# Performance work log

Hardware: AMD Instinct MI355X
Metric: run time of the kernel (lower is better)

The kernel has to match this reference:

```python
import jax, jax.numpy as jnp
import numpy as np

N = 100000   # num_nodes
R = 8        # num_relations
D = 64       # hidden_dim
E = 3200000  # num_edges


def setup_inputs() -> dict:
    key = jax.random.key(0)
    ks = jax.random.split(key, 10)
    s = 1.0 / np.sqrt(D)
    return {
        "x": jnp.arange(N, dtype=jnp.int64),
        "edge_index": jax.random.randint(ks[0], (2, E), 0, N, dtype=jnp.int64),
        "edge_type": jax.random.randint(ks[1], (E,), 0, R, dtype=jnp.int64),
        "emb": jax.random.normal(ks[2], (N, D), dtype=jnp.float32),
        "W1": jax.random.normal(ks[3], (R, D, D), dtype=jnp.float32) * s,
        "root1": jax.random.normal(ks[4], (D, D), dtype=jnp.float32) * s,
        "b1": jnp.zeros((D,), dtype=jnp.float32),
        "W2": jax.random.normal(ks[5], (R, D, D), dtype=jnp.float32) * s,
        "root2": jax.random.normal(ks[6], (D, D), dtype=jnp.float32) * s,
        "b2": jnp.zeros((D,), dtype=jnp.float32),
    }


def rgcn_conv(h, W, root, b, src, dst, etype):
    # per-edge gather of source features: [E, D]
    msgs = h[src]
    # composite segment id: (dst, relation) -> dst * R + relation
    seg = dst * R + etype
    sums = jax.ops.segment_sum(msgs, seg, num_segments=N * R)          # [N*R, D]
    cnt = jax.ops.segment_sum(jnp.ones((msgs.shape[0],), h.dtype), seg,
                              num_segments=N * R)                       # [N*R]
    mean = sums / jnp.maximum(cnt, 1.0)[:, None]                        # per-relation mean aggr
    mean = mean.reshape(N, R, D)
    # relation-specific transform + root weight + bias
    return jnp.einsum('nrd,rde->ne', mean, W) + h @ root + b


def reference(x, edge_index, edge_type, emb, W1, root1, b1, W2, root2, b2):
    src, dst = edge_index[0], edge_index[1]
    h = emb[x]                                   # embedding lookup
    h = rgcn_conv(h, W1, root1, b1, src, dst, edge_type)
    h = jax.nn.relu(h)                           # dropout = identity (eval mode)
    h = rgcn_conv(h, W2, root2, b2, src, dst, edge_type)
    return h
```

## Files before the change

kernel.cpp:

```cpp
#include <hip/hip_runtime.h>

#define N_NODES 100000
#define R_REL   8
#define D_DIM   64
#define E_EDGES 3200000
#define NSEG    (N_NODES * R_REL)
#define NB      782
#define SEG_PER_BKT 1024
#define BKT_CAP 4800
#define P1_BLOCKS 512
#define P1_CHUNK  (E_EDGES / P1_BLOCKS)

typedef __attribute__((ext_vector_type(8))) short short8;
typedef __attribute__((ext_vector_type(4))) float f32x4;

__device__ __forceinline__ unsigned short f2bf(float f) {
    unsigned u = __float_as_uint(f);
    u += 0x7fffu + ((u >> 16) & 1u);
    return (unsigned short)(u >> 16);
}

__device__ __forceinline__ int epack(int s, int d, int r) {
    return (s << 10) | ((d & 127) << 3) | r;
}

__global__ void __launch_bounds__(256)
cvt_kernel(const float* __restrict__ in, unsigned short* __restrict__ outb) {
    size_t base = ((size_t)blockIdx.x * 256 + threadIdx.x) * 8;
    float4 v0 = *(const float4*)(in + base);
    float4 v1 = *(const float4*)(in + base + 4);
    uint4 o;
    o.x = f2bf(v0.x) | ((unsigned)f2bf(v0.y) << 16);
    o.y = f2bf(v0.z) | ((unsigned)f2bf(v0.w) << 16);
    o.z = f2bf(v1.x) | ((unsigned)f2bf(v1.y) << 16);
    o.w = f2bf(v1.z) | ((unsigned)f2bf(v1.w) << 16);
    *(uint4*)(outb + base) = o;
}

__global__ void init_cursor_kernel(int* __restrict__ bkt_cursor) {
    int t = blockIdx.x * 256 + threadIdx.x;
    if (t <= NB) bkt_cursor[t] = t * BKT_CAP;
}

__global__ void __launch_bounds__(256)
p1_scatter_kernel(const int* __restrict__ src, const int* __restrict__ dst,
                  const int* __restrict__ et, int* __restrict__ bkt_cursor,
                  int* __restrict__ packed) {
    __shared__ int hist[NB];
    __shared__ int cur[NB];
    int t = threadIdx.x;
    for (int i = t; i < NB; i += 256) hist[i] = 0;
    __syncthreads();
    int base = blockIdx.x * P1_CHUNK;
    for (int i = t; i < P1_CHUNK; i += 256)
        atomicAdd(&hist[dst[base + i] >> 7], 1);
    __syncthreads();
    for (int i = t; i < NB; i += 256) {
        int c = hist[i];
        cur[i] = c ? atomicAdd(&bkt_cursor[i], c) : 0;
    }
    __syncthreads();
    for (int i = t; i < P1_CHUNK; i += 256) {
        int e = base + i;
        int d = dst[e];
        int pos = atomicAdd(&cur[d >> 7], 1);
        packed[pos] = epack(src[e], d, et[e]);
    }
}

__global__ void __launch_bounds__(256)
p2_sort_kernel(const int* __restrict__ packed, const int* __restrict__ bkt_cursor,
               int* __restrict__ starts, int* __restrict__ ends, int* __restrict__ esrc) {
    __shared__ int shist[SEG_PER_BKT];
    __shared__ int scur[SEG_PER_BKT];
    __shared__ int stmp[256];
    int b = blockIdx.x;
    int t = threadIdx.x;
    int ebase = b * BKT_CAP;
    int eend  = bkt_cursor[b];
    int segbase = b * SEG_PER_BKT;
    int nseg = NSEG - segbase; if (nseg > SEG_PER_BKT) nseg = SEG_PER_BKT;
#pragma unroll
    for (int i = 0; i < 4; ++i) shist[t + i * 256] = 0;
    __syncthreads();
    for (int e = ebase + t; e < eend; e += 256)
        atomicAdd(&shist[packed[e] & 1023], 1);
    __syncthreads();
    int loc[4], s = 0;
    int b4 = t * 4;
#pragma unroll
    for (int i = 0; i < 4; ++i) { loc[i] = shist[b4 + i]; s += loc[i]; }
    stmp[t] = s;
    __syncthreads();
    for (int off = 1; off < 256; off <<= 1) {
        int x = (t >= off) ? stmp[t - off] : 0;
        __syncthreads();
        stmp[t] += x;
        __syncthreads();
    }
    int run = (t == 0) ? 0 : stmp[t - 1];
#pragma unroll
    for (int i = 0; i < 4; ++i) {
        shist[b4 + i] = run; scur[b4 + i] = run;
        run += loc[i];
    }
    __syncthreads();
    for (int i = t; i < nseg; i += 256)
        starts[segbase + i] = ebase + shist[i];
    for (int e = ebase + t; e < eend; e += 256) {
        int p = packed[e];
        int r = atomicAdd(&scur[p & 1023], 1);
        esrc[ebase + r] = p >> 10;
    }
    __syncthreads();
    for (int i = t; i < nseg; i += 256)
        ends[segbase + i] = ebase + scur[i];
}

__global__ void wprep_kernel(const float* __restrict__ W, const float* __restrict__ root,
                             unsigned short* __restrict__ wbuf) {
    int r = blockIdx.x;
    const float* src = (r < 8) ? (W + (size_t)r * 4096) : root;
    __shared__ float t[64][65];
    int a = threadIdx.x >> 2, c = threadIdx.x & 3;
#pragma unroll
    for (int i = 0; i < 4; ++i) {
        float4 v = *(const float4*)(src + a * 64 + c * 16 + i * 4);
        t[a][c * 16 + i * 4 + 0] = v.x;
        t[a][c * 16 + i * 4 + 1] = v.y;
        t[a][c * 16 + i * 4 + 2] = v.z;
        t[a][c * 16 + i * 4 + 3] = v.w;
    }
    __syncthreads();
    unsigned short* outrow = wbuf + (size_t)r * 4096 + a * 64;
#pragma unroll
    for (int i = 0; i < 4; ++i) {
        int k0 = c * 16 + i * 4;
        ushort4 o;
        o.x = f2bf(t[k0 + 0][a]); o.y = f2bf(t[k0 + 1][a]);
        o.z = f2bf(t[k0 + 2][a]); o.w = f2bf(t[k0 + 3][a]);
        *(ushort4*)(outrow + k0) = o;
    }
}

__global__ void __launch_bounds__(512, 6)
fused_kernel(const unsigned short* __restrict__ hb, const int* __restrict__ esrc,
             const int* __restrict__ starts, const int* __restrict__ ends,
             const unsigned short* __restrict__ wbuf, const float* __restrict__ bias,
             void* __restrict__ out, int mode) {
    __shared__ unsigned short As[8][32][72];
    int tid = threadIdx.x;
    int g   = tid >> 4;
    int ml  = tid & 15;
    int n0  = blockIdx.x * 32;

    {
        int segb = (n0 + g) * R_REL;
        int4 eA = *(const int4*)(ends + segb);
        int4 eB = *(const int4*)(ends + segb + 4);
        int beg_cur = starts[segb];
        int end_cur = eA.x;
        int eN = eB.w;
        int r = 0;
        float a0 = 0.f, a1 = 0.f, a2 = 0.f, a3 = 0.f;

#define FLUSH()                                                          \
    do {                                                                 \
        float inv = 1.0f / fmaxf((float)(end_cur - beg_cur), 1.0f);      \
        ushort4 o;                                                       \
        o.x = f2bf(a0 * inv); o.y = f2bf(a1 * inv);                      \
        o.z = f2bf(a2 * inv); o.w = f2bf(a3 * inv);                      \
        *(ushort4*)(&As[r][g][ml * 4]) = o;                              \
        a0 = a1 = a2 = a3 = 0.f;                                         \
        ++r;                                                             \
        beg_cur = end_cur;                                               \
        end_cur = (r == 1) ? eA.y : (r == 2) ? eA.z : (r == 3) ? eA.w :  \
                  (r == 4) ? eB.x : (r == 5) ? eB.y : (r == 6) ? eB.z :  \
                  (r == 7) ? eB.w : 0x7fffffff;                          \
    } while (0)

        int e = beg_cur;
        while (e < eN) {
            int m = eN - e; if (m > 8) m = 8;
            int ids[8];
#pragma unroll
            for (int i = 0; i < 8; ++i) ids[i] = esrc[e + (i < m ? i : 0)];
            uint2 rows[8];
#pragma unroll
            for (int i = 0; i < 8; ++i)
                rows[i] = *(const uint2*)(hb + (size_t)ids[i] * D_DIM + ml * 4);
#pragma unroll
            for (int i = 0; i < 8; ++i) {
                if (i < m) {
                    while (e + i >= end_cur) FLUSH();
                    a0 += __uint_as_float(rows[i].x << 16);
                    a1 += __uint_as_float(rows[i].x & 0xffff0000u);
                    a2 += __uint_as_float(rows[i].y << 16);
                    a3 += __uint_as_float(rows[i].y & 0xffff0000u);
                }
            }
            e += m;
        }
        while (r < 8) FLUSH();
#undef FLUSH
    }

    int w  = tid >> 6;
    int kg = g & 3;
    int h  = w & 1;
    int q  = w >> 1;

    const unsigned short* rp = hb + (size_t)(n0 + h * 16 + ml) * D_DIM + kg * 8;
    short8 RA0 = *(const short8*)(rp);
    short8 RA1 = *(const short8*)(rp + 32);

    __syncthreads();

    f32x4 acc = {0, 0, 0, 0};
#pragma unroll 1
    for (int p = 0; p < 8; ++p) {
        short8 A0 = *(const short8*)(&As[p][h * 16 + ml][kg * 8]);
        short8 A1 = *(const short8*)(&As[p][h * 16 + ml][kg * 8 + 32]);
        const unsigned short* bp = wbuf + (size_t)p * 4096 + (q * 16 + ml) * 64 + kg * 8;
        short8 B0 = *(const short8*)(bp);
        short8 B1 = *(const short8*)(bp + 32);
        acc = __builtin_amdgcn_mfma_f32_16x16x32_bf16(A0, B0, acc, 0, 0, 0);
        acc = __builtin_amdgcn_mfma_f32_16x16x32_bf16(A1, B1, acc, 0, 0, 0);
    }
    {
        const unsigned short* bp = wbuf + (size_t)8 * 4096 + (q * 16 + ml) * 64 + kg * 8;
        short8 B0 = *(const short8*)(bp);
        short8 B1 = *(const short8*)(bp + 32);
        acc = __builtin_amdgcn_mfma_f32_16x16x32_bf16(RA0, B0, acc, 0, 0, 0);
        acc = __builtin_amdgcn_mfma_f32_16x16x32_bf16(RA1, B1, acc, 0, 0, 0);
    }

    float bv = bias[q * 16 + ml];
#pragma unroll
    for (int rg = 0; rg < 4; ++rg) {
        int node = n0 + h * 16 + kg * 4 + rg;
        float v = acc[rg] + bv;
        if (mode) {
            v = fmaxf(v, 0.f);
            ((unsigned short*)out)[(size_t)node * D_DIM + q * 16 + ml] = f2bf(v);
        } else {
            ((float*)out)[(size_t)node * D_DIM + q * 16 + ml] = v;
        }
    }
}


extern "C" void kernel_launch(void* const* d_in, const int* in_sizes, int n_in,
                              void* d_out, int out_size, void* d_ws, size_t ws_size,
                              hipStream_t stream) {
    const int*   ei    = (const int*)d_in[1];
    const int*   src   = ei;
    const int*   dst   = ei + E_EDGES;
    const int*   et    = (const int*)d_in[2];
    const float* emb   = (const float*)d_in[3];
    const float* W1    = (const float*)d_in[4];
    const float* root1 = (const float*)d_in[5];
    const float* b1    = (const float*)d_in[6];
    const float* W2    = (const float*)d_in[7];
    const float* root2 = (const float*)d_in[8];
    const float* b2    = (const float*)d_in[9];
    float*       out   = (float*)d_out;

    unsigned short* embb   = (unsigned short*)d_ws;
    unsigned short* h1b    = embb + (size_t)N_NODES * D_DIM;
    unsigned short* wbuf1  = h1b + (size_t)N_NODES * D_DIM;
    unsigned short* wbuf2  = wbuf1 + 9 * 4096;
    int*            starts = (int*)(wbuf2 + 9 * 4096);
    int*            ends   = starts + NSEG;
    int*            packed = ends + NSEG;
    int*            esrc   = packed + (size_t)NB * BKT_CAP;
    int*            bkt_cursor = esrc + (size_t)NB * BKT_CAP;

    init_cursor_kernel<<<4, 256, 0, stream>>>(bkt_cursor);
    p1_scatter_kernel <<<P1_BLOCKS, 256, 0, stream>>>(src, dst, et, bkt_cursor, packed);
    p2_sort_kernel    <<<NB, 256, 0, stream>>>(packed, bkt_cursor, starts, ends, esrc);

    wprep_kernel<<<9, 256, 0, stream>>>(W1, root1, wbuf1);
    wprep_kernel<<<9, 256, 0, stream>>>(W2, root2, wbuf2);
    cvt_kernel<<<(N_NODES * D_DIM) / 2048, 256, 0, stream>>>(emb, embb);

    const int blocks = N_NODES / 32;

    fused_kernel<<<blocks, 512, 0, stream>>>(embb, esrc, starts, ends, wbuf1, b1, h1b, 1);
    fused_kernel<<<blocks, 512, 0, stream>>>(h1b, esrc, starts, ends, wbuf2, b2, out, 0);
}
```

Measured before the change: 441.0 us.

## Double-buffer edge gathers, stage bucket sort in LDS, vectorize scatter loads

The aggregation loop now software-pipelines its neighbour gathers with two register buffers: the next 8 edge ids and rows are loaded while the current 8 are accumulated. Out-of-range lanes are handled by clamping the index and masking with an FMA instead of a branch. The bucket sort keeps each bucket's packed edges in LDS so the second pass does not re-read global memory. The scatter pass reads src/dst/type as int4 with a different block/chunk split, and the mean reciprocal uses the hardware approximate rcp. The trade-offs are higher register pressure from the double buffers, a few wasted padded loads per node, and slightly less exact division.

```diff
diff --git a/kernel.cpp b/kernel.cpp
--- a/kernel.cpp
+++ b/kernel.cpp
@@ -8,8 +8,8 @@
 #define NB      782
 #define SEG_PER_BKT 1024
 #define BKT_CAP 4800
-#define P1_BLOCKS 512
-#define P1_CHUNK  (E_EDGES / P1_BLOCKS)
+#define P1_BLOCKS 625
+#define P1_CHUNK  5120
 
 typedef __attribute__((ext_vector_type(8))) short short8;
 typedef __attribute__((ext_vector_type(4))) float f32x4;
@@ -52,39 +52,51 @@
     for (int i = t; i < NB; i += 256) hist[i] = 0;
     __syncthreads();
     int base = blockIdx.x * P1_CHUNK;
-    for (int i = t; i < P1_CHUNK; i += 256)
-        atomicAdd(&hist[dst[base + i] >> 7], 1);
+    for (int i = t * 4; i < P1_CHUNK; i += 1024) {
+        int4 d4 = *(const int4*)(dst + base + i);
+        atomicAdd(&hist[d4.x >> 7], 1);
+        atomicAdd(&hist[d4.y >> 7], 1);
+        atomicAdd(&hist[d4.z >> 7], 1);
+        atomicAdd(&hist[d4.w >> 7], 1);
+    }
     __syncthreads();
     for (int i = t; i < NB; i += 256) {
         int c = hist[i];
         cur[i] = c ? atomicAdd(&bkt_cursor[i], c) : 0;
     }
     __syncthreads();
-    for (int i = t; i < P1_CHUNK; i += 256) {
-        int e = base + i;
-        int d = dst[e];
-        int pos = atomicAdd(&cur[d >> 7], 1);
-        packed[pos] = epack(src[e], d, et[e]);
+    for (int i = t * 4; i < P1_CHUNK; i += 1024) {
+        int4 s4 = *(const int4*)(src + base + i);
+        int4 d4 = *(const int4*)(dst + base + i);
+        int4 t4 = *(const int4*)(et  + base + i);
+        int p0 = atomicAdd(&cur[d4.x >> 7], 1); packed[p0] = epack(s4.x, d4.x, t4.x);
+        int p1 = atomicAdd(&cur[d4.y >> 7], 1); packed[p1] = epack(s4.y, d4.y, t4.y);
+        int p2 = atomicAdd(&cur[d4.z >> 7], 1); packed[p2] = epack(s4.z, d4.z, t4.z);
+        int p3 = atomicAdd(&cur[d4.w >> 7], 1); packed[p3] = epack(s4.w, d4.w, t4.w);
     }
 }
 
 __global__ void __launch_bounds__(256)
 p2_sort_kernel(const int* __restrict__ packed, const int* __restrict__ bkt_cursor,
                int* __restrict__ starts, int* __restrict__ ends, int* __restrict__ esrc) {
+    __shared__ int spk[BKT_CAP];
     __shared__ int shist[SEG_PER_BKT];
     __shared__ int scur[SEG_PER_BKT];
     __shared__ int stmp[256];
     int b = blockIdx.x;
     int t = threadIdx.x;
     int ebase = b * BKT_CAP;
-    int eend  = bkt_cursor[b];
+    int ecnt  = bkt_cursor[b] - ebase;
     int segbase = b * SEG_PER_BKT;
     int nseg = NSEG - segbase; if (nseg > SEG_PER_BKT) nseg = SEG_PER_BKT;
 #pragma unroll
     for (int i = 0; i < 4; ++i) shist[t + i * 256] = 0;
     __syncthreads();
-    for (int e = ebase + t; e < eend; e += 256)
-        atomicAdd(&shist[packed[e] & 1023], 1);
+    for (int i = t; i < ecnt; i += 256) {
+        int p = packed[ebase + i];
+        spk[i] = p;
+        atomicAdd(&shist[p & 1023], 1);
+    }
     __syncthreads();
     int loc[4], s = 0;
     int b4 = t * 4;
@@ -107,8 +119,8 @@
     __syncthreads();
     for (int i = t; i < nseg; i += 256)
         starts[segbase + i] = ebase + shist[i];
-    for (int e = ebase + t; e < eend; e += 256) {
-        int p = packed[e];
+    for (int i = t; i < ecnt; i += 256) {
+        int p = spk[i];
         int r = atomicAdd(&scur[p & 1023], 1);
         esrc[ebase + r] = p >> 10;
     }
@@ -166,7 +178,8 @@
 
 #define FLUSH()                                                          \
     do {                                                                 \
-        float inv = 1.0f / fmaxf((float)(end_cur - beg_cur), 1.0f);      \
+        float inv = __builtin_amdgcn_rcpf(                               \
+            fmaxf((float)(end_cur - beg_cur), 1.0f));                    \
         ushort4 o;                                                       \
         o.x = f2bf(a0 * inv); o.y = f2bf(a1 * inv);                      \
         o.z = f2bf(a2 * inv); o.w = f2bf(a3 * inv);                      \
@@ -179,30 +192,51 @@
                   (r == 7) ? eB.w : 0x7fffffff;                          \
     } while (0)
 
-        int e = beg_cur;
-        while (e < eN) {
-            int m = eN - e; if (m > 8) m = 8;
-            int ids[8];
-#pragma unroll
-            for (int i = 0; i < 8; ++i) ids[i] = esrc[e + (i < m ? i : 0)];
-            uint2 rows[8];
-#pragma unroll
-            for (int i = 0; i < 8; ++i)
-                rows[i] = *(const uint2*)(hb + (size_t)ids[i] * D_DIM + ml * 4);
-#pragma unroll
-            for (int i = 0; i < 8; ++i) {
-                if (i < m) {
-                    while (e + i >= end_cur) FLUSH();
-                    a0 += __uint_as_float(rows[i].x << 16);
-                    a1 += __uint_as_float(rows[i].x & 0xffff0000u);
-                    a2 += __uint_as_float(rows[i].y << 16);
-                    a3 += __uint_as_float(rows[i].y & 0xffff0000u);
-                }
+#define LOAD8(IDS, ROWS, EB)                                             \
+    do {                                                                 \
+        _Pragma("unroll")                                                \
+        for (int i = 0; i < 8; ++i) {                                    \
+            int ee = (EB) + i; ee = (ee < eN) ? ee : (eN - 1);           \
+            IDS[i] = esrc[ee];                                           \
+        }                                                                \
+        _Pragma("unroll")                                                \
+        for (int i = 0; i < 8; ++i)                                      \
+            ROWS[i] = *(const uint2*)(hb + (size_t)IDS[i] * D_DIM + ml * 4); \
+    } while (0)
+
+#define ACC8(ROWS, EB)                                                   \
+    do {                                                                 \
+        _Pragma("unroll")                                                \
+        for (int i = 0; i < 8; ++i) {                                    \
+            while ((EB) + i >= end_cur) FLUSH();                         \
+            float msk = ((EB) + i < eN) ? 1.0f : 0.0f;                   \
+            a0 = fmaf(msk, __uint_as_float(ROWS[i].x << 16), a0);        \
+            a1 = fmaf(msk, __uint_as_float(ROWS[i].x & 0xffff0000u), a1);\
+            a2 = fmaf(msk, __uint_as_float(ROWS[i].y << 16), a2);        \
+            a3 = fmaf(msk, __uint_as_float(ROWS[i].y & 0xffff0000u), a3);\
+        }                                                                \
+    } while (0)
+
+        int idsA[8], idsB[8];
+        uint2 rowsA[8], rowsB[8];
+        if (beg_cur < eN) {
+            int e = beg_cur;
+            LOAD8(idsA, rowsA, e);
+            while (true) {
+                LOAD8(idsB, rowsB, e + 8);
+                ACC8(rowsA, e);
+                e += 8;
+                if (e >= eN) break;
+                LOAD8(idsA, rowsA, e + 8);
+                ACC8(rowsB, e);
+                e += 8;
+                if (e >= eN) break;
             }
-            e += m;
         }
         while (r < 8) FLUSH();
 #undef FLUSH
+#undef LOAD8
+#undef ACC8
     }
 
     int w  = tid >> 6;
```

Result: no change. 444.5 us (+0.8%).
